# Optimization experiments

Measured on AMD Instinct MI355X. Metric: run time of the kernel, lower is better.

Reference implementation:

```python
import jax, jax.numpy as jnp
import numpy as np

RADIUS = 0.1
K = 32  # num_neighbors


def _ball_query(points, centers, radius, k):
    # points: [B,3,N], centers: [B,3,M] -> indices [B,M,K] (int32)
    # PVCNN semantics: first k point indices within radius of each center,
    # unfilled slots padded with the first in-ball index (0 if none in ball).
    N = points.shape[-1]
    p2 = jnp.sum(points * points, axis=1)            # [B,N]
    c2 = jnp.sum(centers * centers, axis=1)          # [B,M]
    cp = jnp.einsum('bdm,bdn->bmn', centers, points)  # [B,M,N]
    dist2 = c2[:, :, None] + p2[:, None, :] - 2.0 * cp
    valid = dist2 < radius * radius                  # [B,M,N]
    # score = point index if in ball else sentinel N; sorting ascending puts
    # the first k in-ball indices (in original point order) up front.
    scores = jnp.where(valid, jnp.arange(N, dtype=jnp.int32), jnp.int32(N))
    idx = jnp.sort(scores, axis=-1)[..., :k]         # [B,M,K]
    first = idx[..., :1]
    first = jnp.where(first == N, 0, first)          # no neighbor -> index 0
    return jnp.where(idx == N, first, idx)


def _group(feat, idx):
    # feat: [B,C,N], idx: [B,M,K] -> [B,C,M,K]
    return jnp.take_along_axis(feat[:, :, None, :], idx[:, None, :, :], axis=3)


def setup_inputs() -> dict:
    key = jax.random.key(0)
    k1, k2, k3 = jax.random.split(key, 3)
    B, N, M, C = 2, 16384, 4096, 32
    points_coords = jax.random.uniform(k1, (B, 3, N), dtype=jnp.float32)
    centers_coords = jax.random.uniform(k2, (B, 3, M), dtype=jnp.float32)
    points_features = jax.random.normal(k3, (B, C, N), dtype=jnp.float32)
    return {
        'points_coords': points_coords,
        'centers_coords': centers_coords,
        'points_features': points_features,
    }


def reference(points_coords, centers_coords, points_features):
    idx = _ball_query(points_coords, centers_coords, RADIUS, K)     # [B,M,K]
    nbr_coords = _group(points_coords, idx)                          # [B,3,M,K]
    nbr_coords = nbr_coords - centers_coords[:, :, :, None]         # relative
    nbr_feats = _group(points_features, idx)                         # [B,C,M,K]
    out = jnp.concatenate([nbr_coords, nbr_feats], axis=1)          # [B,3+C,M,K]
    return jnp.transpose(out, (0, 1, 3, 2))                          # [B,3+C,K,M]
```

## Files before the change

kernel.cpp:

```cpp
#include <hip/hip_runtime.h>

#define B_SZ  2
#define N_PTS 16384
#define M_CTR 4096
#define C_FT  32
#define K_NB  32
#define NCH   35
#define CH_STRIDE (K_NB * M_CTR)
#define CELLS 10
#define NCELL (CELLS * CELLS * CELLS)
#define NCHUNK 16
#define BQ_BLOCKS ((B_SZ * M_CTR) / 4)
#define TR_BLOCKS ((B_SZ * N_PTS) / 64)

typedef float vfloat2 __attribute__((ext_vector_type(2)));

__device__ __forceinline__ float fmul(float a, float b) {
    float r; asm("v_mul_f32 %0, %1, %2" : "=v"(r) : "v"(a), "v"(b)); return r;
}
__device__ __forceinline__ float fadd(float a, float b) {
    float r; asm("v_add_f32 %0, %1, %2" : "=v"(r) : "v"(a), "v"(b)); return r;
}
__device__ __forceinline__ float fsub(float a, float b) {
    float r; asm("v_sub_f32 %0, %1, %2" : "=v"(r) : "v"(a), "v"(b)); return r;
}
__device__ __forceinline__ float ffma(float a, float b, float c) {
    float r; asm("v_fma_f32 %0, %1, %2, %3" : "=v"(r) : "v"(a), "v"(b), "v"(c));
    return r;
}

__device__ __forceinline__ bool bq_valid(float x, float y, float z,
                                         float cx, float cy, float cz,
                                         float c2, float r2) {
    const float p2 = fadd(fadd(fmul(x, x), fmul(y, y)), fmul(z, z));
    const float cp = ffma(cz, z, ffma(cy, y, fmul(cx, x)));
    return fsub(fadd(c2, p2), fmul(2.0f, cp)) < r2;
}

__device__ __forceinline__ int cell_of(float x, float y, float z) {
    int ci = (int)(x * 10.0f); ci = ci < 0 ? 0 : (ci > 9 ? 9 : ci);
    int cj = (int)(y * 10.0f); cj = cj < 0 ? 0 : (cj > 9 ? 9 : cj);
    int ck = (int)(z * 10.0f); ck = ck < 0 ? 0 : (ck > 9 ? 9 : ck);
    return (ck * CELLS + cj) * CELLS + ci;
}

__global__ __launch_bounds__(1024) void prep_kernel(
    const float* __restrict__ points,
    int* __restrict__ ghist)
{
    __shared__ int h[NCELL];
    const int t = threadIdx.x;
    const int b = blockIdx.x >> 4;
    const int q = blockIdx.x & (NCHUNK - 1);
    for (int c = t; c < NCELL; c += 1024) h[c] = 0;
    __syncthreads();
    const int n = q * 1024 + t;
    const float x = points[(b * 3 + 0) * N_PTS + n];
    const float y = points[(b * 3 + 1) * N_PTS + n];
    const float z = points[(b * 3 + 2) * N_PTS + n];
    atomicAdd(&h[cell_of(x, y, z)], 1);
    __syncthreads();
    int* __restrict__ g = ghist + (b * NCHUNK + q) * NCELL;
    for (int c = t; c < NCELL; c += 1024) g[c] = h[c];
}

__global__ __launch_bounds__(256) void scatter_kernel(
    const float* __restrict__ points,
    const int* __restrict__ ghist,
    int* __restrict__ starts,
    float4* __restrict__ binned)
{
    const int t = threadIdx.x;
    const int lane = t & 63, wid = t >> 6;
    const int b = blockIdx.x >> 4;
    const int q = blockIdx.x & (NCHUNK - 1);

    __shared__ int curs[NCELL];
    __shared__ int wsum[4];

    const int c0 = 4 * t;
    int tot[4] = {0, 0, 0, 0};
    int pre[4] = {0, 0, 0, 0};
    if (c0 < NCELL) {
        const int* __restrict__ gb = ghist + b * NCHUNK * NCELL;
#pragma unroll
        for (int qq = 0; qq < NCHUNK; ++qq) {
            const int4 v = *(const int4*)&gb[qq * NCELL + c0];
            tot[0] += v.x; tot[1] += v.y; tot[2] += v.z; tot[3] += v.w;
            if (qq < q) { pre[0] += v.x; pre[1] += v.y;
                          pre[2] += v.z; pre[3] += v.w; }
        }
    }
    const int s = tot[0] + tot[1] + tot[2] + tot[3];
    int incl = s;
    for (int off = 1; off < 64; off <<= 1) {
        const int u = __shfl_up(incl, off);
        if (lane >= off) incl += u;
    }
    if (lane == 63) wsum[wid] = incl;
    __syncthreads();
    if (t == 0) {
        int acc = 0;
        for (int w2 = 0; w2 < 4; ++w2) {
            const int x = wsum[w2]; wsum[w2] = acc; acc += x;
        }
    }
    __syncthreads();
    if (c0 < NCELL) {
        int e = incl - s + wsum[wid];
#pragma unroll
        for (int i = 0; i < 4; ++i) {
            if (q == 0) starts[b * (NCELL + 1) + c0 + i] = e;
            curs[c0 + i] = e + pre[i];
            e += tot[i];
        }
        if (q == 0 && c0 + 4 == NCELL)
            starts[b * (NCELL + 1) + NCELL] = e;
    }
    __syncthreads();

    const float* __restrict__ px = points + (b * 3 + 0) * N_PTS;
    const float* __restrict__ py = points + (b * 3 + 1) * N_PTS;
    const float* __restrict__ pz = points + (b * 3 + 2) * N_PTS;
    float4* __restrict__ bb = binned + b * N_PTS;
#pragma unroll
    for (int i = 0; i < 4; ++i) {
        const int n = q * 1024 + i * 256 + t;
        const float x = px[n], y = py[n], z = pz[n];
        const int pos = atomicAdd(&curs[cell_of(x, y, z)], 1);
        bb[pos] = make_float4(x, y, z, __int_as_float(n));
    }
}

__global__ __launch_bounds__(256) void ball_query_kernel(
    const float4* __restrict__ binned,
    const float* __restrict__ centers,
    const int* __restrict__ starts,
    const float* __restrict__ points,
    const float* __restrict__ feats,
    float* __restrict__ pf,
    int* __restrict__ idx_out)
{
    __shared__ union {
        unsigned bitmap[4][N_PTS / 32];
        float    tile[64][37];
    } sh;
    const int t = threadIdx.x;

    if (blockIdx.x >= BQ_BLOCKS) {
        const int tid = blockIdx.x - BQ_BLOCKS;
        const int jb = tid >> 8;
        const int n0 = (tid & 255) * 64;
        for (int i = t; i < NCH * 64; i += 256) {
            const int r = i >> 6;
            const int c = i & 63;
            float v;
            if (r < 3) v = points[(jb * 3 + r) * N_PTS + n0 + c];
            else       v = feats[(jb * C_FT + (r - 3)) * N_PTS + n0 + c];
            sh.tile[c][r] = v;
        }
        if (t < 64) sh.tile[t][35] = 0.0f;
        __syncthreads();
        float* __restrict__ dst = pf + ((size_t)jb * N_PTS + n0) * 36;
        for (int o = t; o < 64 * 36; o += 256) {
            const int c = o / 36;
            const int r = o - c * 36;
            dst[o] = sh.tile[c][r];
        }
        return;
    }

    const int lane = t & 63;
    const int wid  = t >> 6;
    const int cid  = blockIdx.x * 4 + wid;
    const int b = cid >> 12;
    const int m = cid & (M_CTR - 1);

    const float r2 = (float)(0.1 * 0.1);

    const float cx = centers[(b * 3 + 0) * M_CTR + m];
    const float cy = centers[(b * 3 + 1) * M_CTR + m];
    const float cz = centers[(b * 3 + 2) * M_CTR + m];
    const float c2 = fadd(fadd(fmul(cx, cx), fmul(cy, cy)), fmul(cz, cz));

    unsigned* bm = sh.bitmap[wid];
#pragma unroll
    for (int j = 0; j < 8; ++j) bm[j * 64 + lane] = 0u;

    int ci = (int)(cx * 10.0f); ci = ci < 0 ? 0 : (ci > 9 ? 9 : ci);
    int cj = (int)(cy * 10.0f); cj = cj < 0 ? 0 : (cj > 9 ? 9 : cj);
    int ck = (int)(cz * 10.0f); ck = ck < 0 ? 0 : (ck > 9 ? 9 : ck);
    ci = __builtin_amdgcn_readfirstlane(ci);
    cj = __builtin_amdgcn_readfirstlane(cj);
    ck = __builtin_amdgcn_readfirstlane(ck);
    const int i0 = ci > 0 ? ci - 1 : 0;
    const int i1 = ci < 9 ? ci + 1 : 9;
    const int* st = starts + b * (NCELL + 1);
    const float4* __restrict__ bp = binned + b * N_PTS;

    int lo_d[9], hi_d[9];
#pragma unroll
    for (int d = 0; d < 9; ++d) {
        const int jj = cj + (d % 3) - 1;
        const int kk = ck + (d / 3) - 1;
        const bool ok = (jj >= 0) & (jj <= 9) & (kk >= 0) & (kk <= 9);
        const int base = ok ? (kk * CELLS + jj) * CELLS : 0;
        const int lo = st[base + i0];
        const int hi = st[base + i1 + 1];
        lo_d[d] = ok ? lo : 0;
        hi_d[d] = ok ? hi : 0;
    }

#pragma unroll
    for (int d = 0; d < 9; ++d) {
        const int lo = lo_d[d];
        const int hi = hi_d[d];
        for (int s0 = lo; s0 < hi; s0 += 64) {
            const int tt = s0 + lane;
            if (tt < hi) {
                const float4 p = bp[tt];
                if (bq_valid(p.x, p.y, p.z, cx, cy, cz, c2, r2)) {
                    const int n = __float_as_int(p.w);
                    atomicOr((int*)&bm[(((n >> 5) & 7) << 6) + (n >> 8)],
                             1 << (n & 31));
                }
            }
        }
    }

    unsigned w[8];
    int cnt = 0;
#pragma unroll
    for (int j = 0; j < 8; ++j) {
        w[j] = bm[j * 64 + lane];
        cnt += __popc(w[j]);
    }

    int incl = cnt;
    for (int off = 1; off < 64; off <<= 1) {
        const int v = __shfl_up(incl, off);
        if (lane >= off) incl += v;
    }
    const int total = __shfl(incl, 63);
    int slot = incl - cnt;

    int firstbit = 0x7fffffff;
#pragma unroll
    for (int j = 0; j < 8; ++j) {
        if (w[j] && firstbit == 0x7fffffff)
            firstbit = lane * 256 + j * 32 + (__ffs(w[j]) - 1);
    }
    for (int off = 32; off > 0; off >>= 1)
        firstbit = min(firstbit, __shfl_xor(firstbit, off));
    const int first_idx = (total == 0) ? 0 : firstbit;

    int* __restrict__ dst = idx_out + (b * K_NB) * M_CTR + m;
#pragma unroll
    for (int j = 0; j < 8; ++j) {
        unsigned x = w[j];
        while (x && slot < K_NB) {
            const int bit = __ffs(x) - 1;
            dst[slot * M_CTR] = lane * 256 + j * 32 + bit;
            x &= x - 1;
            ++slot;
        }
    }
    if (lane >= total && lane < K_NB) dst[lane * M_CTR] = first_idx;
}

__global__ __launch_bounds__(256) void gather_kernel(
    const float* __restrict__ pf,
    const float* __restrict__ centers,
    const int* __restrict__ idx,
    float* __restrict__ out)
{
    const int t = blockIdx.x * 256 + threadIdx.x;
    const int m = (t & (M_CTR / 2 - 1)) * 2;
    const int k = (t >> 11) & (K_NB - 1);
    const int b = t >> 16;

    const int2 nn = *(const int2*)&idx[(b * K_NB + k) * M_CTR + m];
    const float4* __restrict__ s0 =
        (const float4*)(pf + ((size_t)b * N_PTS + nn.x) * 36);
    const float4* __restrict__ s1 =
        (const float4*)(pf + ((size_t)b * N_PTS + nn.y) * 36);

    float4 f0[9], f1[9];
#pragma unroll
    for (int i = 0; i < 9; ++i) { f0[i] = s0[i]; f1[i] = s1[i]; }

    const float2 cx = *(const float2*)&centers[(b * 3 + 0) * M_CTR + m];
    const float2 cy = *(const float2*)&centers[(b * 3 + 1) * M_CTR + m];
    const float2 cz = *(const float2*)&centers[(b * 3 + 2) * M_CTR + m];

    float v0[36], v1[36];
#pragma unroll
    for (int i = 0; i < 9; ++i) {
        v0[4 * i + 0] = f0[i].x; v0[4 * i + 1] = f0[i].y;
        v0[4 * i + 2] = f0[i].z; v0[4 * i + 3] = f0[i].w;
        v1[4 * i + 0] = f1[i].x; v1[4 * i + 1] = f1[i].y;
        v1[4 * i + 2] = f1[i].z; v1[4 * i + 3] = f1[i].w;
    }
    v0[0] -= cx.x; v0[1] -= cy.x; v0[2] -= cz.x;
    v1[0] -= cx.y; v1[1] -= cy.y; v1[2] -= cz.y;

    float* __restrict__ o = out + ((size_t)b * NCH * K_NB + k) * M_CTR + m;
#pragma unroll
    for (int ch = 0; ch < NCH; ++ch) {
        vfloat2 pv; pv.x = v0[ch]; pv.y = v1[ch];
        __builtin_nontemporal_store(pv, (vfloat2*)&o[(size_t)ch * CH_STRIDE]);
    }
}

extern "C" void kernel_launch(void* const* d_in, const int* in_sizes, int n_in,
                              void* d_out, int out_size, void* d_ws, size_t ws_size,
                              hipStream_t stream) {
    const float* points  = (const float*)d_in[0];
    const float* centers = (const float*)d_in[1];
    const float* feats   = (const float*)d_in[2];
    float* out = (float*)d_out;

    char* ws = (char*)d_ws;
    int*    idx    = (int*)ws;
    float*  pf     = (float*)(ws + (1u << 20));
    int*    ghist  = (int*)(ws + 5636 * 1024);
    int*    starts = (int*)(ws + 5764 * 1024);
    float4* binned = (float4*)(ws + 5776 * 1024);

    prep_kernel<<<B_SZ * NCHUNK, 1024, 0, stream>>>(points, ghist);
    scatter_kernel<<<B_SZ * NCHUNK, 256, 0, stream>>>(
        points, ghist, starts, binned);
    ball_query_kernel<<<BQ_BLOCKS + TR_BLOCKS, 256, 0, stream>>>(
        binned, centers, starts, points, feats, pf, idx);
    gather_kernel<<<(B_SZ * K_NB * M_CTR / 2) / 256, 256, 0, stream>>>(
        pf, centers, idx, out);
}
```

Before: 99.76 us.

## Fuse ball query with gather and merge scatter with feature transpose

The feature transpose moves into the scatter kernel, and the ball-query and gather stages become one kernel. Each 512-thread block handles 8 centers and keeps the neighbor indices in shared memory, so the global idx buffer and one launch go away. The cost is that the gather part now stores a single float per thread, where before it wrote float2 pairs for adjacent centers. Only 256 of 512 threads do the gather, and the larger bitmap shared array may reduce occupancy.

After: 120.3 us. 1.21x slower.

```diff
diff --git a/kernel.cpp b/kernel.cpp
--- a/kernel.cpp
+++ b/kernel.cpp
@@ -10,8 +10,9 @@
 #define CELLS 10
 #define NCELL (CELLS * CELLS * CELLS)
 #define NCHUNK 16
-#define BQ_BLOCKS ((B_SZ * M_CTR) / 4)
+#define SC_BLOCKS (B_SZ * NCHUNK)
 #define TR_BLOCKS ((B_SZ * N_PTS) / 64)
+#define BG_WAVES 8
 
 typedef float vfloat2 __attribute__((ext_vector_type(2)));
 
@@ -64,91 +65,22 @@
     for (int c = t; c < NCELL; c += 1024) g[c] = h[c];
 }
 
-__global__ __launch_bounds__(256) void scatter_kernel(
+__global__ __launch_bounds__(256) void scatter_transpose_kernel(
     const float* __restrict__ points,
+    const float* __restrict__ feats,
     const int* __restrict__ ghist,
     int* __restrict__ starts,
-    float4* __restrict__ binned)
-{
-    const int t = threadIdx.x;
-    const int lane = t & 63, wid = t >> 6;
-    const int b = blockIdx.x >> 4;
-    const int q = blockIdx.x & (NCHUNK - 1);
-
-    __shared__ int curs[NCELL];
-    __shared__ int wsum[4];
-
-    const int c0 = 4 * t;
-    int tot[4] = {0, 0, 0, 0};
-    int pre[4] = {0, 0, 0, 0};
-    if (c0 < NCELL) {
-        const int* __restrict__ gb = ghist + b * NCHUNK * NCELL;
-#pragma unroll
-        for (int qq = 0; qq < NCHUNK; ++qq) {
-            const int4 v = *(const int4*)&gb[qq * NCELL + c0];
-            tot[0] += v.x; tot[1] += v.y; tot[2] += v.z; tot[3] += v.w;
-            if (qq < q) { pre[0] += v.x; pre[1] += v.y;
-                          pre[2] += v.z; pre[3] += v.w; }
-        }
-    }
-    const int s = tot[0] + tot[1] + tot[2] + tot[3];
-    int incl = s;
-    for (int off = 1; off < 64; off <<= 1) {
-        const int u = __shfl_up(incl, off);
-        if (lane >= off) incl += u;
-    }
-    if (lane == 63) wsum[wid] = incl;
-    __syncthreads();
-    if (t == 0) {
-        int acc = 0;
-        for (int w2 = 0; w2 < 4; ++w2) {
-            const int x = wsum[w2]; wsum[w2] = acc; acc += x;
-        }
-    }
-    __syncthreads();
-    if (c0 < NCELL) {
-        int e = incl - s + wsum[wid];
-#pragma unroll
-        for (int i = 0; i < 4; ++i) {
-            if (q == 0) starts[b * (NCELL + 1) + c0 + i] = e;
-            curs[c0 + i] = e + pre[i];
-            e += tot[i];
-        }
-        if (q == 0 && c0 + 4 == NCELL)
-            starts[b * (NCELL + 1) + NCELL] = e;
-    }
-    __syncthreads();
-
-    const float* __restrict__ px = points + (b * 3 + 0) * N_PTS;
-    const float* __restrict__ py = points + (b * 3 + 1) * N_PTS;
-    const float* __restrict__ pz = points + (b * 3 + 2) * N_PTS;
-    float4* __restrict__ bb = binned + b * N_PTS;
-#pragma unroll
-    for (int i = 0; i < 4; ++i) {
-        const int n = q * 1024 + i * 256 + t;
-        const float x = px[n], y = py[n], z = pz[n];
-        const int pos = atomicAdd(&curs[cell_of(x, y, z)], 1);
-        bb[pos] = make_float4(x, y, z, __int_as_float(n));
-    }
-}
-
-__global__ __launch_bounds__(256) void ball_query_kernel(
-    const float4* __restrict__ binned,
-    const float* __restrict__ centers,
-    const int* __restrict__ starts,
-    const float* __restrict__ points,
-    const float* __restrict__ feats,
-    float* __restrict__ pf,
-    int* __restrict__ idx_out)
+    float4* __restrict__ binned,
+    float* __restrict__ pf)
 {
     __shared__ union {
-        unsigned bitmap[4][N_PTS / 32];
-        float    tile[64][37];
+        struct { int curs[NCELL]; int wsum[4]; } sc;
+        float tile[64][37];
     } sh;
     const int t = threadIdx.x;
 
-    if (blockIdx.x >= BQ_BLOCKS) {
-        const int tid = blockIdx.x - BQ_BLOCKS;
+    if (blockIdx.x >= SC_BLOCKS) {
+        const int tid = blockIdx.x - SC_BLOCKS;
         const int jb = tid >> 8;
         const int n0 = (tid & 255) * 64;
         for (int i = t; i < NCH * 64; i += 256) {
@@ -170,145 +102,206 @@
         return;
     }
 
+    const int lane = t & 63, wid = t >> 6;
+    const int b = blockIdx.x >> 4;
+    const int q = blockIdx.x & (NCHUNK - 1);
+
+    const int c0 = 4 * t;
+    int tot[4] = {0, 0, 0, 0};
+    int pre[4] = {0, 0, 0, 0};
+    if (c0 < NCELL) {
+        const int* __restrict__ gb = ghist + b * NCHUNK * NCELL;
+#pragma unroll
+        for (int qq = 0; qq < NCHUNK; ++qq) {
+            const int4 v = *(const int4*)&gb[qq * NCELL + c0];
+            tot[0] += v.x; tot[1] += v.y; tot[2] += v.z; tot[3] += v.w;
+            if (qq < q) { pre[0] += v.x; pre[1] += v.y;
+                          pre[2] += v.z; pre[3] += v.w; }
+        }
+    }
+    const int s = tot[0] + tot[1] + tot[2] + tot[3];
+    int incl = s;
+    for (int off = 1; off < 64; off <<= 1) {
+        const int u = __shfl_up(incl, off);
+        if (lane >= off) incl += u;
+    }
+    if (lane == 63) sh.sc.wsum[wid] = incl;
+    __syncthreads();
+    if (t == 0) {
+        int acc = 0;
+        for (int w2 = 0; w2 < 4; ++w2) {
+            const int x = sh.sc.wsum[w2]; sh.sc.wsum[w2] = acc; acc += x;
+        }
+    }
+    __syncthreads();
+    if (c0 < NCELL) {
+        int e = incl - s + sh.sc.wsum[wid];
+#pragma unroll
+        for (int i = 0; i < 4; ++i) {
+            if (q == 0) starts[b * (NCELL + 1) + c0 + i] = e;
+            sh.sc.curs[c0 + i] = e + pre[i];
+            e += tot[i];
+        }
+        if (q == 0 && c0 + 4 == NCELL)
+            starts[b * (NCELL + 1) + NCELL] = e;
+    }
+    __syncthreads();
+
+    const float* __restrict__ px = points + (b * 3 + 0) * N_PTS;
+    const float* __restrict__ py = points + (b * 3 + 1) * N_PTS;
+    const float* __restrict__ pz = points + (b * 3 + 2) * N_PTS;
+    float4* __restrict__ bb = binned + b * N_PTS;
+#pragma unroll
+    for (int i = 0; i < 4; ++i) {
+        const int n = q * 1024 + i * 256 + t;
+        const float x = px[n], y = py[n], z = pz[n];
+        const int pos = atomicAdd(&sh.sc.curs[cell_of(x, y, z)], 1);
+        bb[pos] = make_float4(x, y, z, __int_as_float(n));
+    }
+}
+
+__global__ __launch_bounds__(512, 4) void bq_gather_kernel(
+    const float4* __restrict__ binned,
+    const float* __restrict__ centers,
+    const int* __restrict__ starts,
+    const float* __restrict__ pf,
+    float* __restrict__ out)
+{
+    __shared__ unsigned bitmap[BG_WAVES][N_PTS / 32];
+    __shared__ int lidx[BG_WAVES][K_NB + 1];
+    const int t = threadIdx.x;
     const int lane = t & 63;
     const int wid  = t >> 6;
-    const int cid  = blockIdx.x * 4 + wid;
+    const int cid  = blockIdx.x * BG_WAVES + wid;
     const int b = cid >> 12;
     const int m = cid & (M_CTR - 1);
 
-    const float r2 = (float)(0.1 * 0.1);
-
-    const float cx = centers[(b * 3 + 0) * M_CTR + m];
-    const float cy = centers[(b * 3 + 1) * M_CTR + m];
-    const float cz = centers[(b * 3 + 2) * M_CTR + m];
-    const float c2 = fadd(fadd(fmul(cx, cx), fmul(cy, cy)), fmul(cz, cz));
-
-    unsigned* bm = sh.bitmap[wid];
-#pragma unroll
-    for (int j = 0; j < 8; ++j) bm[j * 64 + lane] = 0u;
-
-    int ci = (int)(cx * 10.0f); ci = ci < 0 ? 0 : (ci > 9 ? 9 : ci);
-    int cj = (int)(cy * 10.0f); cj = cj < 0 ? 0 : (cj > 9 ? 9 : cj);
-    int ck = (int)(cz * 10.0f); ck = ck < 0 ? 0 : (ck > 9 ? 9 : ck);
-    ci = __builtin_amdgcn_readfirstlane(ci);
-    cj = __builtin_amdgcn_readfirstlane(cj);
-    ck = __builtin_amdgcn_readfirstlane(ck);
-    const int i0 = ci > 0 ? ci - 1 : 0;
-    const int i1 = ci < 9 ? ci + 1 : 9;
-    const int* st = starts + b * (NCELL + 1);
-    const float4* __restrict__ bp = binned + b * N_PTS;
-
-    int lo_d[9], hi_d[9];
-#pragma unroll
-    for (int d = 0; d < 9; ++d) {
-        const int jj = cj + (d % 3) - 1;
-        const int kk = ck + (d / 3) - 1;
-        const bool ok = (jj >= 0) & (jj <= 9) & (kk >= 0) & (kk <= 9);
-        const int base = ok ? (kk * CELLS + jj) * CELLS : 0;
-        const int lo = st[base + i0];
-        const int hi = st[base + i1 + 1];
-        lo_d[d] = ok ? lo : 0;
-        hi_d[d] = ok ? hi : 0;
-    }
-
-#pragma unroll
-    for (int d = 0; d < 9; ++d) {
-        const int lo = lo_d[d];
-        const int hi = hi_d[d];
-        for (int s0 = lo; s0 < hi; s0 += 64) {
-            const int tt = s0 + lane;
-            if (tt < hi) {
-                const float4 p = bp[tt];
-                if (bq_valid(p.x, p.y, p.z, cx, cy, cz, c2, r2)) {
-                    const int n = __float_as_int(p.w);
-                    atomicOr((int*)&bm[(((n >> 5) & 7) << 6) + (n >> 8)],
-                             1 << (n & 31));
+    {
+        const float r2 = (float)(0.1 * 0.1);
+
+        const float cx = centers[(b * 3 + 0) * M_CTR + m];
+        const float cy = centers[(b * 3 + 1) * M_CTR + m];
+        const float cz = centers[(b * 3 + 2) * M_CTR + m];
+        const float c2 = fadd(fadd(fmul(cx, cx), fmul(cy, cy)), fmul(cz, cz));
+
+        unsigned* bm = bitmap[wid];
+#pragma unroll
+        for (int j = 0; j < 8; ++j) bm[j * 64 + lane] = 0u;
+
+        int ci = (int)(cx * 10.0f); ci = ci < 0 ? 0 : (ci > 9 ? 9 : ci);
+        int cj = (int)(cy * 10.0f); cj = cj < 0 ? 0 : (cj > 9 ? 9 : cj);
+        int ck = (int)(cz * 10.0f); ck = ck < 0 ? 0 : (ck > 9 ? 9 : ck);
+        ci = __builtin_amdgcn_readfirstlane(ci);
+        cj = __builtin_amdgcn_readfirstlane(cj);
+        ck = __builtin_amdgcn_readfirstlane(ck);
+        const int i0 = ci > 0 ? ci - 1 : 0;
+        const int i1 = ci < 9 ? ci + 1 : 9;
+        const int* st = starts + b * (NCELL + 1);
+        const float4* __restrict__ bp = binned + b * N_PTS;
+
+        int lo_d[9], hi_d[9];
+#pragma unroll
+        for (int d = 0; d < 9; ++d) {
+            const int jj = cj + (d % 3) - 1;
+            const int kk = ck + (d / 3) - 1;
+            const bool ok = (jj >= 0) & (jj <= 9) & (kk >= 0) & (kk <= 9);
+            const int base = ok ? (kk * CELLS + jj) * CELLS : 0;
+            const int lo = st[base + i0];
+            const int hi = st[base + i1 + 1];
+            lo_d[d] = ok ? lo : 0;
+            hi_d[d] = ok ? hi : 0;
+        }
+
+#pragma unroll
+        for (int d = 0; d < 9; ++d) {
+            const int lo = lo_d[d];
+            const int hi = hi_d[d];
+            for (int s0 = lo; s0 < hi; s0 += 64) {
+                const int tt = s0 + lane;
+                if (tt < hi) {
+                    const float4 p = bp[tt];
+                    if (bq_valid(p.x, p.y, p.z, cx, cy, cz, c2, r2)) {
+                        const int n = __float_as_int(p.w);
+                        atomicOr((int*)&bm[(((n >> 5) & 7) << 6) + (n >> 8)],
+                                 1 << (n & 31));
+                    }
                 }
             }
         }
-    }
-
-    unsigned w[8];
-    int cnt = 0;
-#pragma unroll
-    for (int j = 0; j < 8; ++j) {
-        w[j] = bm[j * 64 + lane];
-        cnt += __popc(w[j]);
-    }
-
-    int incl = cnt;
-    for (int off = 1; off < 64; off <<= 1) {
-        const int v = __shfl_up(incl, off);
-        if (lane >= off) incl += v;
-    }
-    const int total = __shfl(incl, 63);
-    int slot = incl - cnt;
-
-    int firstbit = 0x7fffffff;
-#pragma unroll
-    for (int j = 0; j < 8; ++j) {
-        if (w[j] && firstbit == 0x7fffffff)
-            firstbit = lane * 256 + j * 32 + (__ffs(w[j]) - 1);
-    }
-    for (int off = 32; off > 0; off >>= 1)
-        firstbit = min(firstbit, __shfl_xor(firstbit, off));
-    const int first_idx = (total == 0) ? 0 : firstbit;
-
-    int* __restrict__ dst = idx_out + (b * K_NB) * M_CTR + m;
-#pragma unroll
-    for (int j = 0; j < 8; ++j) {
-        unsigned x = w[j];
-        while (x && slot < K_NB) {
-            const int bit = __ffs(x) - 1;
-            dst[slot * M_CTR] = lane * 256 + j * 32 + bit;
-            x &= x - 1;
-            ++slot;
-        }
-    }
-    if (lane >= total && lane < K_NB) dst[lane * M_CTR] = first_idx;
-}
-
-__global__ __launch_bounds__(256) void gather_kernel(
-    const float* __restrict__ pf,
-    const float* __restrict__ centers,
-    const int* __restrict__ idx,
-    float* __restrict__ out)
-{
-    const int t = blockIdx.x * 256 + threadIdx.x;
-    const int m = (t & (M_CTR / 2 - 1)) * 2;
-    const int k = (t >> 11) & (K_NB - 1);
-    const int b = t >> 16;
-
-    const int2 nn = *(const int2*)&idx[(b * K_NB + k) * M_CTR + m];
-    const float4* __restrict__ s0 =
-        (const float4*)(pf + ((size_t)b * N_PTS + nn.x) * 36);
-    const float4* __restrict__ s1 =
-        (const float4*)(pf + ((size_t)b * N_PTS + nn.y) * 36);
-
-    float4 f0[9], f1[9];
-#pragma unroll
-    for (int i = 0; i < 9; ++i) { f0[i] = s0[i]; f1[i] = s1[i]; }
-
-    const float2 cx = *(const float2*)&centers[(b * 3 + 0) * M_CTR + m];
-    const float2 cy = *(const float2*)&centers[(b * 3 + 1) * M_CTR + m];
-    const float2 cz = *(const float2*)&centers[(b * 3 + 2) * M_CTR + m];
-
-    float v0[36], v1[36];
-#pragma unroll
-    for (int i = 0; i < 9; ++i) {
-        v0[4 * i + 0] = f0[i].x; v0[4 * i + 1] = f0[i].y;
-        v0[4 * i + 2] = f0[i].z; v0[4 * i + 3] = f0[i].w;
-        v1[4 * i + 0] = f1[i].x; v1[4 * i + 1] = f1[i].y;
-        v1[4 * i + 2] = f1[i].z; v1[4 * i + 3] = f1[i].w;
-    }
-    v0[0] -= cx.x; v0[1] -= cy.x; v0[2] -= cz.x;
-    v1[0] -= cx.y; v1[1] -= cy.y; v1[2] -= cz.y;
-
-    float* __restrict__ o = out + ((size_t)b * NCH * K_NB + k) * M_CTR + m;
-#pragma unroll
-    for (int ch = 0; ch < NCH; ++ch) {
-        vfloat2 pv; pv.x = v0[ch]; pv.y = v1[ch];
-        __builtin_nontemporal_store(pv, (vfloat2*)&o[(size_t)ch * CH_STRIDE]);
+
+        unsigned w[8];
+        int cnt = 0;
+#pragma unroll
+        for (int j = 0; j < 8; ++j) {
+            w[j] = bm[j * 64 + lane];
+            cnt += __popc(w[j]);
+        }
+
+        int incl = cnt;
+        for (int off = 1; off < 64; off <<= 1) {
+            const int v = __shfl_up(incl, off);
+            if (lane >= off) incl += v;
+        }
+        const int total = __shfl(incl, 63);
+        int slot = incl - cnt;
+
+        int firstbit = 0x7fffffff;
+#pragma unroll
+        for (int j = 0; j < 8; ++j) {
+            if (w[j] && firstbit == 0x7fffffff)
+                firstbit = lane * 256 + j * 32 + (__ffs(w[j]) - 1);
+        }
+        for (int off = 32; off > 0; off >>= 1)
+            firstbit = min(firstbit, __shfl_xor(firstbit, off));
+        const int first_idx = (total == 0) ? 0 : firstbit;
+
+#pragma unroll
+        for (int j = 0; j < 8; ++j) {
+            unsigned x = w[j];
+            while (x && slot < K_NB) {
+                const int bit = __ffs(x) - 1;
+                lidx[wid][slot] = lane * 256 + j * 32 + bit;
+                x &= x - 1;
+                ++slot;
+            }
+        }
+        if (lane >= total && lane < K_NB) lidx[wid][lane] = first_idx;
+    }
+
+    __syncthreads();
+
+    if (t < BG_WAVES * K_NB) {
+        const int mloc = t & (BG_WAVES - 1);
+        const int k    = t >> 3;
+        const int gcid = blockIdx.x * BG_WAVES + mloc;
+        const int gb = gcid >> 12;
+        const int gm = gcid & (M_CTR - 1);
+        const int n = lidx[mloc][k];
+
+        const float4* __restrict__ src =
+            (const float4*)(pf + ((size_t)gb * N_PTS + n) * 36);
+        float4 f[9];
+#pragma unroll
+        for (int i = 0; i < 9; ++i) f[i] = src[i];
+
+        f[0].x -= centers[(gb * 3 + 0) * M_CTR + gm];
+        f[0].y -= centers[(gb * 3 + 1) * M_CTR + gm];
+        f[0].z -= centers[(gb * 3 + 2) * M_CTR + gm];
+
+        float* __restrict__ o =
+            out + ((size_t)(gb * NCH) * K_NB + k) * M_CTR + gm;
+#pragma unroll
+        for (int i = 0; i < 9; ++i) {
+#pragma unroll
+            for (int j = 0; j < 4; ++j) {
+                const int ch = 4 * i + j;
+                if (ch < NCH) {
+                    const float v = (j == 0) ? f[i].x : (j == 1) ? f[i].y
+                                  : (j == 2) ? f[i].z : f[i].w;
+                    __builtin_nontemporal_store(v, &o[(size_t)ch * CH_STRIDE]);
+                }
+            }
+        }
     }
 }
 
@@ -321,17 +314,14 @@
     float* out = (float*)d_out;
 
     char* ws = (char*)d_ws;
-    int*    idx    = (int*)ws;
     float*  pf     = (float*)(ws + (1u << 20));
     int*    ghist  = (int*)(ws + 5636 * 1024);
     int*    starts = (int*)(ws + 5764 * 1024);
     float4* binned = (float4*)(ws + 5776 * 1024);
 
     prep_kernel<<<B_SZ * NCHUNK, 1024, 0, stream>>>(points, ghist);
-    scatter_kernel<<<B_SZ * NCHUNK, 256, 0, stream>>>(
-        points, ghist, starts, binned);
-    ball_query_kernel<<<BQ_BLOCKS + TR_BLOCKS, 256, 0, stream>>>(
-        binned, centers, starts, points, feats, pf, idx);
-    gather_kernel<<<(B_SZ * K_NB * M_CTR / 2) / 256, 256, 0, stream>>>(
-        pf, centers, idx, out);
-}
+    scatter_transpose_kernel<<<SC_BLOCKS + TR_BLOCKS, 256, 0, stream>>>(
+        points, feats, ghist, starts, binned, pf);
+    bq_gather_kernel<<<(B_SZ * M_CTR) / BG_WAVES, 512, 0, stream>>>(
+        binned, centers, starts, pf, out);
+}
```
